# Kernel optimization log

Hardware: AMD Instinct MI355X
Metric: run time of the kernel (lower is better)

The kernel has to match this reference:

```python
import jax, jax.numpy as jnp
import numpy as np

EPS = 1e-5
NUM_HEADS = 8
KEY_DIM = 16
D = 64  # attn_ratio * key_dim


def conv1x1_bn(x, w, g, b, m, v):
    # x: (B, Cin, H, W), w: (Cout, Cin); eval-mode BatchNorm over channel dim
    y = jnp.einsum('bchw,oc->bohw', x, w)
    scale = (g * jax.lax.rsqrt(v + EPS))[None, :, None, None]
    shift = (b - g * m * jax.lax.rsqrt(v + EPS))[None, :, None, None]
    return y * scale + shift


def setup_inputs() -> dict:
    key = jax.random.key(0)
    ks = jax.random.split(key, 22)
    dim, nh_kd, dh = 384, 128, 512
    f = jax.random.normal
    u = jax.random.uniform
    return {
        'x': f(ks[0], (2, dim, 56, 56), jnp.float32),
        'wq': f(ks[1], (nh_kd, dim), jnp.float32) * 0.05,
        'qg': u(ks[2], (nh_kd,), jnp.float32), 'qb': f(ks[3], (nh_kd,)) * 0.1,
        'qm': f(ks[4], (nh_kd,)) * 0.1, 'qv': u(ks[5], (nh_kd,)) + 0.5,
        'wk': f(ks[6], (nh_kd, dim), jnp.float32) * 0.05,
        'kg': u(ks[7], (nh_kd,), jnp.float32), 'kb': f(ks[8], (nh_kd,)) * 0.1,
        'km': f(ks[9], (nh_kd,)) * 0.1, 'kvv': u(ks[10], (nh_kd,)) + 0.5,
        'wv': f(ks[11], (dh, dim), jnp.float32) * 0.05,
        'vg': u(ks[12], (dh,), jnp.float32), 'vb': f(ks[13], (dh,)) * 0.1,
        'vm': f(ks[14], (dh,)) * 0.1, 'vvv': u(ks[15], (dh,)) + 0.5,
        'wp': f(ks[16], (dim, dh), jnp.float32) * 0.05,
        'pg': u(ks[17], (dim,), jnp.float32), 'pb': f(ks[18], (dim,)) * 0.1,
        'pm': f(ks[19], (dim,)) * 0.1, 'pvv': u(ks[20], (dim,)) + 0.5,
    }


def reference(x, wq, qg, qb, qm, qv, wk, kg, kb, km, kvv,
              wv, vg, vb, vm, vvv, wp, pg, pb, pm, pvv):
    B, C, H, W = x.shape
    N = H * W
    h, kd, d = NUM_HEADS, KEY_DIM, D
    # (B, h, N, kd)
    qq = conv1x1_bn(x, wq, qg, qb, qm, qv).reshape(B, h, kd, N).transpose(0, 1, 3, 2)
    # (B, h, kd, N)
    kk = conv1x1_bn(x, wk, kg, kb, km, kvv).reshape(B, h, kd, N)
    # (B, h, N, d)
    vv = conv1x1_bn(x, wv, vg, vb, vm, vvv).reshape(B, h, d, N).transpose(0, 1, 3, 2)
    # NOTE: original forward does NOT apply self.scale
    attn = jax.nn.softmax(jnp.matmul(qq, kk), axis=-1)  # (B, h, N, N)
    xx = jnp.matmul(attn, vv)                            # (B, h, N, d)
    xx = xx.transpose(0, 1, 3, 2).reshape(B, h * d, H, W)
    xx = jax.nn.relu(xx)
    return conv1x1_bn(xx, wp, pg, pb, pm, pvv)
```

## Files before the change

### kernel.cpp

```cpp
#include <hip/hip_runtime.h>
#include <hip/hip_bf16.h>

#define B_   2
#define CIN  384
#define NPIX 3136
#define NH   8
#define KD   16
#define DHEAD 64
#define NHKD 128
#define QKW  256
#define DHD  512
#define EPSW 1e-5f
#define L2E  1.4426950408889634f

typedef __attribute__((ext_vector_type(8))) short vshort8;
typedef __attribute__((ext_vector_type(4))) short vshort4;
typedef __attribute__((ext_vector_type(4))) float vfloat4;
typedef __attribute__((ext_vector_type(16))) float vfloat16;

#if __has_builtin(__builtin_amdgcn_exp2f)
#define EXP2F __builtin_amdgcn_exp2f
#else
#define EXP2F exp2f
#endif

static __device__ __forceinline__ float bf2f(short s) {
    unsigned int u = ((unsigned int)(unsigned short)s) << 16;
    return __builtin_bit_cast(float, u);
}
static __device__ __forceinline__ short f2bf(float f) {
    unsigned int u = __builtin_bit_cast(unsigned int, f);
    unsigned int lsb = (u >> 16) & 1u;
    u += 0x7fffu + lsb;
    return (short)(u >> 16);
}
static __device__ __forceinline__ float pget(const void* p, int i, int f32) {
    return f32 ? ((const float*)p)[i] : bf2f(((const short*)p)[i]);
}

static __device__ __forceinline__ int detect_f32(const unsigned short* x) {
    int lane = threadIdx.x & 63;
    bool big = false;
#pragma unroll
    for (int j = 0; j < 8; j++) {
        int e = (x[(lane * 8 + j) * 2] >> 7) & 0xFF;
        big = big || (e >= 0xC0);
    }
    unsigned long long bal = __ballot(big);
    return __popcll(bal) >= 32;
}

__global__ __launch_bounds__(256) void prep_kernel(
    const void* __restrict__ x,
    const void* __restrict__ wq, const void* __restrict__ wk,
    const void* __restrict__ wv, const void* __restrict__ wp,
    short* __restrict__ wB, short* __restrict__ xT,
    const void* qg, const void* qb, const void* qm, const void* qv,
    const void* kg, const void* kb, const void* km, const void* kv,
    const void* vg, const void* vb, const void* vm, const void* vv,
    const void* pg, const void* pb, const void* pm, const void* pv,
    float* __restrict__ scA, float* __restrict__ shA)
{
    __shared__ short tile[32][33];
    int f32 = detect_f32((const unsigned short*)x);
    int id = blockIdx.x;
    int t = threadIdx.x;

    if (id < 1920) {
        int i = id * 256 + t;
        const void* src; int j;
        if (i < 49152)       { src = wq; j = i; }
        else if (i < 98304)  { src = wk; j = i - 49152; }
        else if (i < 294912) { src = wv; j = i - 98304; }
        else                 { src = wp; j = i - 294912; }
        wB[i] = f32 ? f2bf(((const float*)src)[j]) : ((const short*)src)[j];
        if (i < 1152) {
            const void *g, *bb, *mn, *vr;
            if (i < 128)      { g = qg; bb = qb; mn = qm; vr = qv; j = i; }
            else if (i < 256) { g = kg; bb = kb; mn = km; vr = kv; j = i - 128; }
            else if (i < 768) { g = vg; bb = vb; mn = vm; vr = vv; j = i - 256; }
            else              { g = pg; bb = pb; mn = pm; vr = pv; j = i - 768; }
            float iv = rsqrtf(pget(vr, j, f32) + EPSW);
            float s = pget(g, j, f32) * iv;
            float h = pget(bb, j, f32) - pget(mn, j, f32) * s;
            if (i < 128) { s *= L2E; h *= L2E; }
            scA[i] = s;
            shA[i] = h;
        }
        return;
    }

    int tid2 = id - 1920;
    int b = tid2 / 1176, rr = tid2 % 1176;
    int n0 = (rr % 98) * 32, c0 = (rr / 98) * 32;
    int r = t >> 3, q4 = (t & 7) * 4;
    size_t off = ((size_t)b * CIN + c0 + r) * NPIX + n0 + q4;
    if (f32) {
        float4 v = *(const float4*)((const float*)x + off);
        tile[r][q4 + 0] = f2bf(v.x);
        tile[r][q4 + 1] = f2bf(v.y);
        tile[r][q4 + 2] = f2bf(v.z);
        tile[r][q4 + 3] = f2bf(v.w);
    } else {
        vshort4 v = *(const vshort4*)((const short*)x + off);
#pragma unroll
        for (int i = 0; i < 4; i++) tile[r][q4 + i] = v[i];
    }
    __syncthreads();
    vshort4 o;
#pragma unroll
    for (int i = 0; i < 4; i++) o[i] = tile[q4 + i][r];
    *(vshort4*)(xT + ((size_t)b * NPIX + n0 + r) * CIN + c0 + q4) = o;
}

static __device__ __forceinline__ void gemm32_body(
    short* Al, short* Bl,
    const short* __restrict__ A, const short* __restrict__ Bt,
    void* __restrict__ C, size_t coff, int m0, int n0,
    const float* __restrict__ sc, const float* __restrict__ sh,
    int Nb, int K, int Mreal, int bnPerRow, int finalOut, int f32)
{
    int t = threadIdx.x, lane = t & 63, w = t >> 6;
    int c31 = lane & 31, half = lane >> 5;
    int arow = t >> 1, ak = (t & 1) * 32;
    int brow = t >> 2, bk = (t & 3) * 16;
    const short* ag = A + (size_t)(m0 + arow) * K + ak;
    const short* bg = Bt + (size_t)(n0 + brow) * K + bk;

    vfloat16 acc0, acc1;
#pragma unroll
    for (int i = 0; i < 16; i++) { acc0[i] = 0.f; acc1[i] = 0.f; }

    for (int k0 = 0; k0 < K; k0 += 64) {
        vshort8 a0 = *(const vshort8*)(ag + k0);
        vshort8 a1 = *(const vshort8*)(ag + k0 + 8);
        vshort8 a2 = *(const vshort8*)(ag + k0 + 16);
        vshort8 a3 = *(const vshort8*)(ag + k0 + 24);
        vshort8 b0 = *(const vshort8*)(bg + k0);
        vshort8 b1 = *(const vshort8*)(bg + k0 + 8);
        __syncthreads();
        *(vshort8*)&Al[arow * 72 + ak]      = a0;
        *(vshort8*)&Al[arow * 72 + ak + 8]  = a1;
        *(vshort8*)&Al[arow * 72 + ak + 16] = a2;
        *(vshort8*)&Al[arow * 72 + ak + 24] = a3;
        *(vshort8*)&Bl[brow * 72 + bk]      = b0;
        *(vshort8*)&Bl[brow * 72 + bk + 8]  = b1;
        __syncthreads();
#pragma unroll
        for (int ks = 0; ks < 4; ks++) {
            vshort8 af  = *(const vshort8*)&Al[(w * 32 + c31) * 72 + ks * 16 + half * 8];
            vshort8 bf0 = *(const vshort8*)&Bl[(c31) * 72 + ks * 16 + half * 8];
            vshort8 bf1 = *(const vshort8*)&Bl[(32 + c31) * 72 + ks * 16 + half * 8];
            acc0 = __builtin_amdgcn_mfma_f32_32x32x16_bf16(af, bf0, acc0, 0, 0, 0);
            acc1 = __builtin_amdgcn_mfma_f32_32x32x16_bf16(af, bf1, acc1, 0, 0, 0);
        }
    }

#pragma unroll
    for (int cb = 0; cb < 2; cb++) {
        int col = n0 + cb * 32 + c31;
        float scc = bnPerRow ? 0.f : sc[col];
        float shc = bnPerRow ? 0.f : sh[col];
#pragma unroll
        for (int r = 0; r < 16; r++) {
            int rowl = (r & 3) + 8 * (r >> 2) + 4 * half;
            int row = m0 + w * 32 + rowl;
            if (row >= Mreal) continue;
            float s2 = bnPerRow ? sc[row] : scc;
            float h2 = bnPerRow ? sh[row] : shc;
            float v = cb ? acc1[r] : acc0[r];
            float val = s2 * v + h2;
            size_t idx = coff + (size_t)row * Nb + col;
            if (finalOut && f32) ((float*)C)[idx] = val;
            else                 ((short*)C)[idx] = f2bf(val);
        }
    }
}

__global__ __launch_bounds__(256) void proj_kernel(
    const short* __restrict__ xT, const short* __restrict__ wqkB,
    const short* __restrict__ wvB, short* __restrict__ QKt,
    short* __restrict__ Vb,
    const float* __restrict__ scA, const float* __restrict__ shA)
{
    __shared__ __attribute__((aligned(16))) short Al[128 * 72];
    __shared__ __attribute__((aligned(16))) short Bl[64 * 72];
    int id = blockIdx.x;
    if (id < 200) {
        int b = id / 100, r = id % 100;
        int m0 = (r % 25) * 128, n0 = (r / 25) * 64;
        gemm32_body(Al, Bl, xT + (size_t)b * NPIX * CIN, wqkB,
                    QKt, (size_t)b * NPIX * QKW, m0, n0,
                    scA, shA, QKW, CIN, NPIX, 0, 0, 0);
    } else {
        id -= 200;
        int b = id / 196, r = id % 196;
        int m0 = (r / 49) * 128, n0 = (r % 49) * 64;
        gemm32_body(Al, Bl, wvB, xT + (size_t)b * NPIX * CIN,
                    Vb, (size_t)b * DHD * NPIX, m0, n0,
                    scA + 256, shA + 256, NPIX, CIN, DHD, 1, 0, 0);
    }
}

__global__ __launch_bounds__(256) void pgemm_kernel(
    const short* __restrict__ wpB, const short* __restrict__ xx,
    void* __restrict__ out,
    const float* __restrict__ scA, const float* __restrict__ shA,
    const void* __restrict__ x)
{
    __shared__ __attribute__((aligned(16))) short Al[128 * 72];
    __shared__ __attribute__((aligned(16))) short Bl[64 * 72];
    int f32 = detect_f32((const unsigned short*)x);
    int id = blockIdx.x;
    int b = id / 147, r = id % 147;
    int m0 = (r / 49) * 128, n0 = (r % 49) * 64;
    gemm32_body(Al, Bl, wpB, xx + (size_t)b * NPIX * DHD,
                out, (size_t)b * CIN * NPIX, m0, n0,
                scA + 768, shA + 768, NPIX, DHD, CIN, 1, 1, f32);
}

__global__ __launch_bounds__(128) void attn_kernel(
    const short* __restrict__ QKt, const short* __restrict__ V,
    short* __restrict__ xx)
{
    __shared__ __attribute__((aligned(16))) short Kl[2][64 * 16];
    __shared__ __attribute__((aligned(16))) short Vl[2][64 * 72];
    __shared__ __attribute__((aligned(16))) short Pl[64 * 72];
    int bh = blockIdx.y, b = bh >> 3, h = bh & 7;
    int q0 = blockIdx.x * 64;
    int t = threadIdx.x, lane = t & 63, w = t >> 6;
    int c31 = lane & 31, half = lane >> 5;

    int q = q0 + w * 32 + c31;
    vshort8 aq = *(const vshort8*)(QKt + ((size_t)b * NPIX + q) * QKW + h * KD + half * 8);

    vfloat16 o0, o1, oL, z16;
#pragma unroll
    for (int i = 0; i < 16; i++) { o0[i] = 0.f; o1[i] = 0.f; oL[i] = 0.f; z16[i] = 0.f; }

    int kkey = t >> 1, kofs = (t & 1) * 8;
    const short* kgp = QKt + (size_t)b * NPIX * QKW + NHKD + h * KD + kofs;
    int vd = t >> 1, vkh = (t & 1) * 32;
    const short* vgp = V + ((size_t)(b * DHD) + h * DHEAD + vd) * NPIX + vkh;
    const short one_bf = (short)0x3F80;
    const vshort8 ones = {one_bf, one_bf, one_bf, one_bf, one_bf, one_bf, one_bf, one_bf};

    *(vshort8*)&Kl[0][kkey * 16 + kofs] = *(const vshort8*)(kgp + (size_t)kkey * QKW);
#pragma unroll
    for (int i = 0; i < 4; i++)
        *(vshort8*)&Vl[0][vd * 72 + vkh + i * 8] = *(const vshort8*)(vgp + i * 8);
    __syncthreads();

    for (int it = 0; it < NPIX / 64; ++it) {
        int cur = it & 1, nxt = cur ^ 1;
        int k0 = it * 64;
        bool more = (it + 1) < (NPIX / 64);
        vshort8 ks, vs[4];
        if (more) {
            ks = *(const vshort8*)(kgp + (size_t)(k0 + 64 + kkey) * QKW);
#pragma unroll
            for (int i = 0; i < 4; i++)
                vs[i] = *(const vshort8*)(vgp + k0 + 64 + i * 8);
        }

        short* pw = &Pl[(w * 32 + c31) * 72];
#pragma unroll
        for (int kg = 0; kg < 2; kg++) {
            vshort8 ak = *(const vshort8*)&Kl[cur][(kg * 32 + c31) * 16 + half * 8];
            vfloat16 s = __builtin_amdgcn_mfma_f32_32x32x16_bf16(ak, aq, z16, 0, 0, 0);
#pragma unroll
            for (int rb = 0; rb < 4; rb++) {
                vshort4 pv;
#pragma unroll
                for (int j = 0; j < 4; j++) {
                    float p = EXP2F(s[rb * 4 + j]);
                    pv[j] = (short)(__builtin_bit_cast(unsigned int, p) >> 16);
                }
                *(vshort4*)&pw[kg * 32 + half * 4 + rb * 8] = pv;
            }
        }

#pragma unroll
        for (int kc = 0; kc < 4; kc++) {
            vshort8 ap  = *(const vshort8*)&Pl[(w * 32 + c31) * 72 + kc * 16 + half * 8];
            vshort8 bv0 = *(const vshort8*)&Vl[cur][(c31) * 72 + kc * 16 + half * 8];
            vshort8 bv1 = *(const vshort8*)&Vl[cur][(32 + c31) * 72 + kc * 16 + half * 8];
            o0 = __builtin_amdgcn_mfma_f32_32x32x16_bf16(ap, bv0, o0, 0, 0, 0);
            o1 = __builtin_amdgcn_mfma_f32_32x32x16_bf16(ap, bv1, o1, 0, 0, 0);
            oL = __builtin_amdgcn_mfma_f32_32x32x16_bf16(ap, ones, oL, 0, 0, 0);
        }

        if (more) {
            *(vshort8*)&Kl[nxt][kkey * 16 + kofs] = ks;
#pragma unroll
            for (int i = 0; i < 4; i++)
                *(vshort8*)&Vl[nxt][vd * 72 + vkh + i * 8] = vs[i];
        }
        __syncthreads();
    }

#pragma unroll
    for (int r = 0; r < 16; r++) {
        int ql = (r & 3) + 8 * (r >> 2) + 4 * half;
        int qrow = q0 + w * 32 + ql;
        float inv = 1.0f / oL[r];
        size_t base = ((size_t)b * NPIX + qrow) * DHD + h * DHEAD + c31;
        xx[base]      = f2bf(fmaxf(o0[r] * inv, 0.f));
        xx[base + 32] = f2bf(fmaxf(o1[r] * inv, 0.f));
    }
}

extern "C" void kernel_launch(void* const* d_in, const int* in_sizes, int n_in,
                              void* d_out, int out_size, void* d_ws, size_t ws_size,
                              hipStream_t stream) {
    const void* x  = d_in[0];
    const void* wq = d_in[1];
    const void* qg = d_in[2];  const void* qb = d_in[3];
    const void* qm = d_in[4];  const void* qv = d_in[5];
    const void* wk = d_in[6];
    const void* kg = d_in[7];  const void* kb = d_in[8];
    const void* km = d_in[9];  const void* kv = d_in[10];
    const void* wv = d_in[11];
    const void* vg = d_in[12]; const void* vb = d_in[13];
    const void* vm = d_in[14]; const void* vv = d_in[15];
    const void* wp = d_in[16];
    const void* pg = d_in[17]; const void* pb = d_in[18];
    const void* pm = d_in[19]; const void* pv = d_in[20];

    short* xT  = (short*)d_ws;
    short* wB  = xT + (size_t)B_ * NPIX * CIN;
    short* wqkB = wB;
    short* wvB  = wB + 98304;
    short* wpB  = wB + 294912;
    short* QKt = wB + 491520;
    short* Vb  = QKt + (size_t)B_ * NPIX * QKW;
    short* xx  = Vb + (size_t)B_ * DHD * NPIX;
    float* scA = (float*)(xx + (size_t)B_ * NPIX * DHD);
    float* shA = scA + 1152;

    prep_kernel<<<4272, 256, 0, stream>>>(
        x, wq, wk, wv, wp, wB, xT,
        qg, qb, qm, qv, kg, kb, km, kv,
        vg, vb, vm, vv, pg, pb, pm, pv, scA, shA);

    proj_kernel<<<592, 256, 0, stream>>>(xT, wqkB, wvB, QKt, Vb, scA, shA);

    attn_kernel<<<dim3(NPIX / 64, B_ * NH), 128, 0, stream>>>(QKt, Vb, xx);

    pgemm_kernel<<<294, 256, 0, stream>>>(wpB, xx, d_out, scA, shA, x);
}
```

Measured before the change: 199.5 us.

## Load attention K/V directly from global into registers with single-wave blocks

```diff
diff --git a/kernel.cpp b/kernel.cpp
--- a/kernel.cpp
+++ b/kernel.cpp
@@ -219,90 +219,70 @@
                 scA + 768, shA + 768, NPIX, DHD, CIN, 1, 1, f32);
 }
 
-__global__ __launch_bounds__(128) void attn_kernel(
+__global__ __launch_bounds__(64) void attn_kernel(
     const short* __restrict__ QKt, const short* __restrict__ V,
     short* __restrict__ xx)
 {
-    __shared__ __attribute__((aligned(16))) short Kl[2][64 * 16];
-    __shared__ __attribute__((aligned(16))) short Vl[2][64 * 72];
-    __shared__ __attribute__((aligned(16))) short Pl[64 * 72];
+    __shared__ __attribute__((aligned(16))) short Pl[32 * 72];
     int bh = blockIdx.y, b = bh >> 3, h = bh & 7;
-    int q0 = blockIdx.x * 64;
-    int t = threadIdx.x, lane = t & 63, w = t >> 6;
-    int c31 = lane & 31, half = lane >> 5;
-
-    int q = q0 + w * 32 + c31;
-    vshort8 aq = *(const vshort8*)(QKt + ((size_t)b * NPIX + q) * QKW + h * KD + half * 8);
+    int q0 = blockIdx.x * 32;
+    int t = threadIdx.x;
+    int c31 = t & 31, half = t >> 5;
+
+    vshort8 aq = *(const vshort8*)(QKt + ((size_t)b * NPIX + q0 + c31) * QKW
+                                   + h * KD + half * 8);
 
     vfloat16 o0, o1, oL, z16;
 #pragma unroll
     for (int i = 0; i < 16; i++) { o0[i] = 0.f; o1[i] = 0.f; oL[i] = 0.f; z16[i] = 0.f; }
 
-    int kkey = t >> 1, kofs = (t & 1) * 8;
-    const short* kgp = QKt + (size_t)b * NPIX * QKW + NHKD + h * KD + kofs;
-    int vd = t >> 1, vkh = (t & 1) * 32;
-    const short* vgp = V + ((size_t)(b * DHD) + h * DHEAD + vd) * NPIX + vkh;
+    const short* kbase = QKt + (size_t)b * NPIX * QKW + NHKD + h * KD + half * 8;
+    const short* vb0 = V + ((size_t)(b * DHD) + h * DHEAD + c31) * NPIX + half * 8;
+    const short* vb1 = vb0 + (size_t)32 * NPIX;
     const short one_bf = (short)0x3F80;
     const vshort8 ones = {one_bf, one_bf, one_bf, one_bf, one_bf, one_bf, one_bf, one_bf};
 
-    *(vshort8*)&Kl[0][kkey * 16 + kofs] = *(const vshort8*)(kgp + (size_t)kkey * QKW);
-#pragma unroll
-    for (int i = 0; i < 4; i++)
-        *(vshort8*)&Vl[0][vd * 72 + vkh + i * 8] = *(const vshort8*)(vgp + i * 8);
-    __syncthreads();
-
-    for (int it = 0; it < NPIX / 64; ++it) {
-        int cur = it & 1, nxt = cur ^ 1;
-        int k0 = it * 64;
-        bool more = (it + 1) < (NPIX / 64);
-        vshort8 ks, vs[4];
-        if (more) {
-            ks = *(const vshort8*)(kgp + (size_t)(k0 + 64 + kkey) * QKW);
-#pragma unroll
-            for (int i = 0; i < 4; i++)
-                vs[i] = *(const vshort8*)(vgp + k0 + 64 + i * 8);
-        }
-
-        short* pw = &Pl[(w * 32 + c31) * 72];
-#pragma unroll
-        for (int kg = 0; kg < 2; kg++) {
-            vshort8 ak = *(const vshort8*)&Kl[cur][(kg * 32 + c31) * 16 + half * 8];
-            vfloat16 s = __builtin_amdgcn_mfma_f32_32x32x16_bf16(ak, aq, z16, 0, 0, 0);
-#pragma unroll
-            for (int rb = 0; rb < 4; rb++) {
-                vshort4 pv;
-#pragma unroll
-                for (int j = 0; j < 4; j++) {
-                    float p = EXP2F(s[rb * 4 + j]);
-                    pv[j] = (short)(__builtin_bit_cast(unsigned int, p) >> 16);
-                }
-                *(vshort4*)&pw[kg * 32 + half * 4 + rb * 8] = pv;
+    short* pw = &Pl[c31 * 72];
+
+    for (int k0 = 0; k0 < NPIX; k0 += 64) {
+        vshort8 ak0 = *(const vshort8*)(kbase + (size_t)(k0 + c31) * QKW);
+        vshort8 ak1 = *(const vshort8*)(kbase + (size_t)(k0 + 32 + c31) * QKW);
+        vshort8 bv0[4], bv1[4];
+#pragma unroll
+        for (int kc = 0; kc < 4; kc++) {
+            bv0[kc] = *(const vshort8*)(vb0 + k0 + kc * 16);
+            bv1[kc] = *(const vshort8*)(vb1 + k0 + kc * 16);
+        }
+
+        vfloat16 s0 = __builtin_amdgcn_mfma_f32_32x32x16_bf16(ak0, aq, z16, 0, 0, 0);
+        vfloat16 s1 = __builtin_amdgcn_mfma_f32_32x32x16_bf16(ak1, aq, z16, 0, 0, 0);
+#pragma unroll
+        for (int rb = 0; rb < 4; rb++) {
+            vshort4 p0, p1;
+#pragma unroll
+            for (int j = 0; j < 4; j++) {
+                float e0 = EXP2F(s0[rb * 4 + j]);
+                float e1 = EXP2F(s1[rb * 4 + j]);
+                p0[j] = (short)(__builtin_bit_cast(unsigned int, e0) >> 16);
+                p1[j] = (short)(__builtin_bit_cast(unsigned int, e1) >> 16);
             }
+            *(vshort4*)&pw[half * 4 + rb * 8]      = p0;
+            *(vshort4*)&pw[32 + half * 4 + rb * 8] = p1;
         }
 
 #pragma unroll
         for (int kc = 0; kc < 4; kc++) {
-            vshort8 ap  = *(const vshort8*)&Pl[(w * 32 + c31) * 72 + kc * 16 + half * 8];
-            vshort8 bv0 = *(const vshort8*)&Vl[cur][(c31) * 72 + kc * 16 + half * 8];
-            vshort8 bv1 = *(const vshort8*)&Vl[cur][(32 + c31) * 72 + kc * 16 + half * 8];
-            o0 = __builtin_amdgcn_mfma_f32_32x32x16_bf16(ap, bv0, o0, 0, 0, 0);
-            o1 = __builtin_amdgcn_mfma_f32_32x32x16_bf16(ap, bv1, o1, 0, 0, 0);
+            vshort8 ap = *(const vshort8*)&Pl[c31 * 72 + kc * 16 + half * 8];
+            o0 = __builtin_amdgcn_mfma_f32_32x32x16_bf16(ap, bv0[kc], o0, 0, 0, 0);
+            o1 = __builtin_amdgcn_mfma_f32_32x32x16_bf16(ap, bv1[kc], o1, 0, 0, 0);
             oL = __builtin_amdgcn_mfma_f32_32x32x16_bf16(ap, ones, oL, 0, 0, 0);
         }
-
-        if (more) {
-            *(vshort8*)&Kl[nxt][kkey * 16 + kofs] = ks;
-#pragma unroll
-            for (int i = 0; i < 4; i++)
-                *(vshort8*)&Vl[nxt][vd * 72 + vkh + i * 8] = vs[i];
-        }
-        __syncthreads();
     }
 
 #pragma unroll
     for (int r = 0; r < 16; r++) {
         int ql = (r & 3) + 8 * (r >> 2) + 4 * half;
-        int qrow = q0 + w * 32 + ql;
+        int qrow = q0 + ql;
         float inv = 1.0f / oL[r];
         size_t base = ((size_t)b * NPIX + qrow) * DHD + h * DHEAD + c31;
         xx[base]      = f2bf(fmaxf(o0[r] * inv, 0.f));
@@ -345,7 +325,7 @@
 
     proj_kernel<<<592, 256, 0, stream>>>(xT, wqkB, wvB, QKt, Vb, scA, shA);
 
-    attn_kernel<<<dim3(NPIX / 64, B_ * NH), 128, 0, stream>>>(QKt, Vb, xx);
+    attn_kernel<<<dim3(NPIX / 32, B_ * NH), 64, 0, stream>>>(QKt, Vb, xx);
 
     pgemm_kernel<<<294, 256, 0, stream>>>(wpB, xx, d_out, scA, shA, x);
 }
```

Measured after the change: 243.2 us. 21.9% more time.
